# Performance work log

Measured on AMD Instinct MI355X. Metric: run time of the kernel, lower is better.

Reference implementation:

```python
import jax, jax.numpy as jnp
import numpy as np

B, L, D = 2, 2048, 2048
H, G, HD = 16, 4, 128
EPS = 1e-6
THETA_BASE = 10000.0


def setup_inputs() -> dict:
    key = jax.random.key(0)
    ks = jax.random.split(key, 5)
    x = jax.random.normal(ks[0], (B, L, D), jnp.float32)
    Wq = jax.random.normal(ks[1], (D, H * HD), jnp.float32) * 0.02
    Wk = jax.random.normal(ks[2], (D, G * HD), jnp.float32) * 0.02
    Wv = jax.random.normal(ks[3], (D, G * HD), jnp.float32) * 0.02
    Wo = jax.random.normal(ks[4], (H * HD, D), jnp.float32) * 0.02
    q_scale = jnp.ones((HD,), jnp.float32)
    k_scale = jnp.ones((HD,), jnp.float32)
    # Well-formed RoPE tables of shape [L, HD] (duplicated-half layout expected by apply_rope)
    inv_freq = 1.0 / (THETA_BASE ** (jnp.arange(0, HD // 2, dtype=jnp.float32) * 2.0 / HD))  # [HD/2]
    angles = jnp.arange(L, dtype=jnp.float32)[:, None] * inv_freq[None, :]  # [L, HD/2]
    angles = jnp.concatenate([angles, angles], axis=1)  # [L, HD]
    cos = jnp.cos(angles)
    sin = jnp.sin(angles)
    # Causal mask: True = masked (matches masked_fill(mask, -inf))
    mask = jnp.triu(jnp.ones((L, L), dtype=bool), k=1)
    return {"x": x, "Wq": Wq, "Wk": Wk, "Wv": Wv, "Wo": Wo,
            "q_scale": q_scale, "k_scale": k_scale, "cos": cos, "sin": sin, "mask": mask}


def _rmsnorm(x, scale):
    var = jnp.mean(x * x, axis=-1, keepdims=True)
    return x * jax.lax.rsqrt(var + EPS) * scale


def _rope(x, cos, sin):
    # x: [B, h, L, HD]; cos/sin: [L, HD]
    hd = x.shape[-1]
    x1, x2 = x[..., : hd // 2], x[..., hd // 2 :]
    rotated = jnp.concatenate([-x2, x1], axis=-1)
    return x * cos[None, None] + rotated * sin[None, None]


def reference(x, Wq, Wk, Wv, Wo, q_scale, k_scale, cos, sin, mask):
    b, l, _ = x.shape
    q = (x @ Wq).reshape(b, l, H, HD).transpose(0, 2, 1, 3)  # [B,H,L,HD]
    k = (x @ Wk).reshape(b, l, G, HD).transpose(0, 2, 1, 3)  # [B,G,L,HD]
    v = (x @ Wv).reshape(b, l, G, HD).transpose(0, 2, 1, 3)
    q = _rmsnorm(q, q_scale)
    k = _rmsnorm(k, k_scale)
    q = _rope(q, cos, sin)
    k = _rope(k, cos, sin)
    gs = H // G
    k = jnp.repeat(k, gs, axis=1)  # [B,H,L,HD]
    v = jnp.repeat(v, gs, axis=1)
    scores = jnp.einsum('bhqd,bhkd->bhqk', q, k)
    scores = jnp.where(mask, -jnp.inf, scores)
    # NB: faithful to the source's unusual scaling by head_dim**2 (not sqrt)
    w = jax.nn.softmax(scores / float(HD ** 2), axis=-1)
    out = jnp.einsum('bhqk,bhkd->bhqd', w, v).transpose(0, 2, 1, 3).reshape(b, l, H * HD)
    return out @ Wo
```

## Files before the change

### kernel.cpp

```cpp
#include <hip/hip_runtime.h>
#include <math.h>

#define SEQ 2048
#define DMODEL 2048
#define NHQ 16
#define NHK 4

typedef __attribute__((ext_vector_type(8))) short short8;
typedef __attribute__((ext_vector_type(8))) unsigned short ushort8;
typedef __attribute__((ext_vector_type(4))) float floatx4;

__device__ __forceinline__ unsigned short f2bf(float f) {
  unsigned int u = __builtin_bit_cast(unsigned int, f);
  u += 0x7fffu + ((u >> 16) & 1u);
  return (unsigned short)(u >> 16);
}
__device__ __forceinline__ float bf2f(unsigned short s) {
  unsigned int u = ((unsigned int)s) << 16;
  return __builtin_bit_cast(float, u);
}

__global__ __launch_bounds__(256) void prep(const float* __restrict__ x,
                                            const float* __restrict__ Wq,
                                            const float* __restrict__ Wk,
                                            const float* __restrict__ Wv,
                                            const float* __restrict__ Wo,
                                            unsigned short* __restrict__ x_bf,
                                            unsigned short* __restrict__ wqkv_t,
                                            unsigned short* __restrict__ wo_t) {
  const int z = blockIdx.z;
  const int tx = threadIdx.x, ty = threadIdx.y;
  const int tid = ty * 32 + tx;
  if (z == 3) {
    const size_t base = ((size_t)(blockIdx.y * 64 + blockIdx.x)) * 4096 + (size_t)tid * 16;
    const float4 v0 = *(const float4*)(x + base);
    const float4 v1 = *(const float4*)(x + base + 4);
    const float4 v2 = *(const float4*)(x + base + 8);
    const float4 v3 = *(const float4*)(x + base + 12);
    ushort8 w0, w1;
    w0[0] = f2bf(v0.x); w0[1] = f2bf(v0.y); w0[2] = f2bf(v0.z); w0[3] = f2bf(v0.w);
    w0[4] = f2bf(v1.x); w0[5] = f2bf(v1.y); w0[6] = f2bf(v1.z); w0[7] = f2bf(v1.w);
    w1[0] = f2bf(v2.x); w1[1] = f2bf(v2.y); w1[2] = f2bf(v2.z); w1[3] = f2bf(v2.w);
    w1[4] = f2bf(v3.x); w1[5] = f2bf(v3.y); w1[6] = f2bf(v3.z); w1[7] = f2bf(v3.w);
    *(ushort8*)(x_bf + base) = w0;
    *(ushort8*)(x_bf + base + 8) = w1;
    return;
  }
  int bx = blockIdx.x;
  const float* in;
  unsigned short* out;
  int C;
  const int R = 2048;
  if (z == 0)      { in = Wq; out = wqkv_t;                          C = 2048; }
  else if (z == 1) { in = Wo; out = wo_t;                            C = 2048; }
  else {
    if (bx < 16)      { in = Wk; out = wqkv_t + (size_t)2048 * 2048; C = 512; }
    else if (bx < 32) { in = Wv; out = wqkv_t + (size_t)2560 * 2048; C = 512; bx -= 16; }
    else return;
  }
  __shared__ float tile[32][65];
  const int c0 = bx * 32, r0 = blockIdx.y * 64;
#pragma unroll
  for (int j = 0; j < 8; ++j)
    tile[tx][ty + j * 8] = in[(size_t)(r0 + ty + j * 8) * C + c0 + tx];
  __syncthreads();
  const int c = tid >> 3;
  const int l8 = tid & 7;
  ushort8 w;
#pragma unroll
  for (int u = 0; u < 8; ++u) w[u] = f2bf(tile[c][l8 * 8 + u]);
  *(ushort8*)(out + (size_t)(c0 + c) * R + r0 + l8 * 8) = w;
}

__device__ __forceinline__ void stage_tile(const unsigned short* __restrict__ A,
                                           const unsigned short* __restrict__ Bt,
                                           unsigned short* As, unsigned short* Bs,
                                           int bm, int bn, int K, int k0,
                                           int wave, int srow, int scol) {
#pragma unroll
  for (int it = 0; it < 2; ++it) {
    const int rowa = wave * 32 + it * 16;
    const unsigned short* ga = A + (size_t)(bm + rowa + srow) * K + k0 + scol;
    const unsigned short* gb = Bt + (size_t)(bn + rowa + srow) * K + k0 + scol;
    __builtin_amdgcn_global_load_lds(
        (const __attribute__((address_space(1))) void*)ga,
        (__attribute__((address_space(3))) void*)&As[rowa * 32], 16, 0, 0);
    __builtin_amdgcn_global_load_lds(
        (const __attribute__((address_space(1))) void*)gb,
        (__attribute__((address_space(3))) void*)&Bs[rowa * 32], 16, 0, 0);
  }
}

__device__ __forceinline__ void mfma_tile(const unsigned short* As, const unsigned short* Bs,
                                          floatx4 (&acc)[4][4],
                                          int wr, int wc, int m15, int quad) {
  short8 af[4], bfr[4];
  const unsigned short* pa = &As[(wr * 64 + m15) * 32 + quad * 8];
  const unsigned short* pb = &Bs[(wc * 64 + m15) * 32 + quad * 8];
#pragma unroll
  for (int i = 0; i < 4; ++i) af[i] = *(const short8*)(pa + i * 16 * 32);
#pragma unroll
  for (int j = 0; j < 4; ++j) bfr[j] = *(const short8*)(pb + j * 16 * 32);
#pragma unroll
  for (int i = 0; i < 4; ++i)
#pragma unroll
    for (int j = 0; j < 4; ++j)
      acc[i][j] = __builtin_amdgcn_mfma_f32_16x16x32_bf16(af[i], bfr[j], acc[i][j], 0, 0, 0);
}

__global__ __launch_bounds__(256) void gemm_qkv_fused(const unsigned short* __restrict__ A,
                                                      const unsigned short* __restrict__ Bt,
                                                      unsigned short* __restrict__ qout,
                                                      unsigned short* __restrict__ kout,
                                                      unsigned short* __restrict__ vout,
                                                      const float* __restrict__ q_scale,
                                                      const float* __restrict__ k_scale,
                                                      const float* __restrict__ cosb,
                                                      const float* __restrict__ sinb) {
  __shared__ unsigned short smem[128 * 129];
  unsigned short* As0 = smem;
  unsigned short* Bs0 = smem + 4096;
  unsigned short* As1 = smem + 8192;
  unsigned short* Bs1 = smem + 12288;

  const int tid = threadIdx.x;
  const int wave = tid >> 6;
  const int lane = tid & 63;
  const int bm = blockIdx.y * 128;
  const int bx = blockIdx.x;
  const int bn = bx * 128;
  const int wr = wave >> 1;
  const int wc = wave & 1;
  const int m15 = lane & 15;
  const int quad = lane >> 4;

  floatx4 acc[4][4];
#pragma unroll
  for (int i = 0; i < 4; ++i)
#pragma unroll
    for (int j = 0; j < 4; ++j) acc[i][j] = (floatx4){0.f, 0.f, 0.f, 0.f};

  const int srow = lane >> 2;
  const int scol = (lane & 3) * 8;

  stage_tile(A, Bt, As0, Bs0, bm, bn, 2048, 0, wave, srow, scol);
  __syncthreads();

  for (int k0 = 0; k0 < 2048; k0 += 64) {
    stage_tile(A, Bt, As1, Bs1, bm, bn, 2048, k0 + 32, wave, srow, scol);
    mfma_tile(As0, Bs0, acc, wr, wc, m15, quad);
    __syncthreads();
    if (k0 + 64 < 2048)
      stage_tile(A, Bt, As0, Bs0, bm, bn, 2048, k0 + 64, wave, srow, scol);
    mfma_tile(As1, Bs1, acc, wr, wc, m15, quad);
    __syncthreads();
  }

#pragma unroll
  for (int i = 0; i < 4; ++i)
#pragma unroll
    for (int j = 0; j < 4; ++j) {
      const int col = wc * 64 + j * 16 + m15;
#pragma unroll
      for (int reg = 0; reg < 4; ++reg) {
        const int row = wr * 64 + i * 16 + quad * 4 + reg;
        smem[row * 129 + col] = f2bf(acc[i][j][reg]);
      }
    }
  __syncthreads();

  const int t = tid & 63;
  const int wv = tid >> 6;
  const int b = bm >> 11;
  const int l_base = bm & (SEQ - 1);

  if (bx < 20) {
    const float* scale = (bx < NHQ) ? q_scale : k_scale;
    unsigned short* dstbase = (bx < NHQ)
        ? qout + ((size_t)(b * NHQ + bx) * SEQ + l_base) * 128
        : kout + ((size_t)(b * NHK + (bx - NHQ)) * SEQ + l_base) * 128;
    const float sc0 = scale[t];
    const float sc1 = scale[t + 64];
#pragma unroll 4
    for (int rr = 0; rr < 32; ++rr) {
      const int row = wv * 32 + rr;
      const float v0 = bf2f(smem[row * 129 + t]);
      const float v1 = bf2f(smem[row * 129 + t + 64]);
      float ss = v0 * v0 + v1 * v1;
#pragma unroll
      for (int m = 1; m < 64; m <<= 1) ss += __shfl_xor(ss, m);
      const float r = rsqrtf(ss * (1.0f / 128.0f) + 1e-6f);
      const int l = l_base + row;
      const float c0 = cosb[(size_t)l * 128 + t];
      const float s0 = sinb[(size_t)l * 128 + t];
      const float c1 = cosb[(size_t)l * 128 + t + 64];
      const float s1 = sinb[(size_t)l * 128 + t + 64];
      const float a0 = v0 * r * sc0;
      const float a1 = v1 * r * sc1;
      unsigned short* dst = dstbase + (size_t)row * 128;
      dst[t]      = f2bf(a0 * c0 - a1 * s0);
      dst[t + 64] = f2bf(a1 * c1 + a0 * s1);
    }
  } else {
    const int g = bx - 20;
    unsigned short* vbase = vout + (size_t)(b * NHK + g) * 128 * SEQ + l_base;
#pragma unroll 4
    for (int dd = 0; dd < 32; ++dd) {
      const int d = wv * 32 + dd;
      unsigned short* dst = vbase + (size_t)d * SEQ;
      dst[t]      = smem[t * 129 + d];
      dst[t + 64] = smem[(t + 64) * 129 + d];
    }
  }
}

__global__ __launch_bounds__(256) void gemm_bf16_f32(const unsigned short* __restrict__ A,
                                                     const unsigned short* __restrict__ Bt,
                                                     float* __restrict__ C,
                                                     int M, int N, int K) {
  __shared__ unsigned short smem[4 * 128 * 32];
  unsigned short* As0 = smem;
  unsigned short* Bs0 = smem + 4096;
  unsigned short* As1 = smem + 8192;
  unsigned short* Bs1 = smem + 12288;

  const int tid = threadIdx.x;
  const int wave = tid >> 6;
  const int lane = tid & 63;
  const int bm = blockIdx.y * 128;
  const int bn = blockIdx.x * 128;
  const int wr = wave >> 1;
  const int wc = wave & 1;
  const int m15 = lane & 15;
  const int quad = lane >> 4;

  floatx4 acc[4][4];
#pragma unroll
  for (int i = 0; i < 4; ++i)
#pragma unroll
    for (int j = 0; j < 4; ++j) acc[i][j] = (floatx4){0.f, 0.f, 0.f, 0.f};

  const int srow = lane >> 2;
  const int scol = (lane & 3) * 8;

  stage_tile(A, Bt, As0, Bs0, bm, bn, K, 0, wave, srow, scol);
  __syncthreads();

  for (int k0 = 0; k0 < K; k0 += 64) {
    stage_tile(A, Bt, As1, Bs1, bm, bn, K, k0 + 32, wave, srow, scol);
    mfma_tile(As0, Bs0, acc, wr, wc, m15, quad);
    __syncthreads();
    if (k0 + 64 < K)
      stage_tile(A, Bt, As0, Bs0, bm, bn, K, k0 + 64, wave, srow, scol);
    mfma_tile(As1, Bs1, acc, wr, wc, m15, quad);
    __syncthreads();
  }

#pragma unroll
  for (int i = 0; i < 4; ++i)
#pragma unroll
    for (int j = 0; j < 4; ++j) {
      const int col = bn + wc * 64 + j * 16 + m15;
#pragma unroll
      for (int reg = 0; reg < 4; ++reg) {
        const int row = bm + wr * 64 + i * 16 + quad * 4 + reg;
        C[(size_t)row * N + col] = acc[i][j][reg];
      }
    }
}

__global__ __launch_bounds__(256, 4) void attn_mfma(const unsigned short* __restrict__ qb,
                                                    const unsigned short* __restrict__ kb,
                                                    const unsigned short* __restrict__ vtb,
                                                    unsigned short* __restrict__ o) {
  __shared__ unsigned short Ks[64 * 128];
  __shared__ unsigned short Vs[128 * 64];
  unsigned short* Ps = Ks;

  const int tid = threadIdx.x;
  const int wave = tid >> 6;
  const int lane = tid & 63;
  const int m15 = lane & 15;
  const int quad = lane >> 4;
  const int bh = blockIdx.x;
  const int b = bh >> 4;
  const int h = bh & 15;
  const int g = h >> 2;
  const int q0 = ((int)gridDim.y - 1 - (int)blockIdx.y) * 64;

  const unsigned short* qhead = qb + (size_t)bh * SEQ * 128;
  const unsigned short* khead = kb + (size_t)(b * NHK + g) * SEQ * 128;
  const unsigned short* vthead = vtb + (size_t)(b * NHK + g) * 128 * SEQ;

  short8 qf[4];
  {
    const unsigned short* qp = qhead + (size_t)(q0 + wave * 16 + m15) * 128 + quad * 8;
#pragma unroll
    for (int ks = 0; ks < 4; ++ks) qf[ks] = *(const short8*)(qp + ks * 32);
  }

  floatx4 acc_o[8];
#pragma unroll
  for (int n = 0; n < 8; ++n) acc_o[n] = (floatx4){0.f, 0.f, 0.f, 0.f};
  float l_lane[4] = {0.f, 0.f, 0.f, 0.f};
  const float inv_scale = 1.0f / 16384.0f;

  for (int j0 = 0; j0 <= q0; j0 += 64) {
#pragma unroll
    for (int t = 0; t < 4; ++t) {
      const int r = wave * 16 + t * 4 + (lane >> 4);
      const int cg = (lane & 15) ^ (r & 15);
      const unsigned short* src = khead + (size_t)(j0 + r) * 128 + cg * 8;
      __builtin_amdgcn_global_load_lds(
          (const __attribute__((address_space(1))) void*)src,
          (__attribute__((address_space(3))) void*)&Ks[(wave * 16 + t * 4) * 128], 16, 0, 0);
    }
#pragma unroll
    for (int t = 0; t < 4; ++t) {
      const int d = wave * 32 + t * 8 + (lane >> 3);
      const int cg = (lane & 7) ^ (d & 7);
      const unsigned short* src = vthead + (size_t)d * SEQ + j0 + cg * 8;
      __builtin_amdgcn_global_load_lds(
          (const __attribute__((address_space(1))) void*)src,
          (__attribute__((address_space(3))) void*)&Vs[(wave * 32 + t * 8) * 64], 16, 0, 0);
    }
    __syncthreads();

    floatx4 acc_s[4];
#pragma unroll
    for (int n = 0; n < 4; ++n) acc_s[n] = (floatx4){0.f, 0.f, 0.f, 0.f};
#pragma unroll
    for (int ks = 0; ks < 4; ++ks) {
#pragma unroll
      for (int n = 0; n < 4; ++n) {
        const short8 bfrag = *(const short8*)&Ks[(n * 16 + m15) * 128 + (((ks * 4 + quad) ^ m15) * 8)];
        acc_s[n] = __builtin_amdgcn_mfma_f32_16x16x32_bf16(qf[ks], bfrag, acc_s[n], 0, 0, 0);
      }
    }
    __syncthreads();

    if (j0 == q0) {
      const int row_g = wave * 16 + quad * 4;
#pragma unroll
      for (int n = 0; n < 4; ++n) {
        const int col = n * 16 + m15;
#pragma unroll
        for (int rg = 0; rg < 4; ++rg) {
          float p = (col > row_g + rg) ? 0.0f : __expf(acc_s[n][rg] * inv_scale);
          l_lane[rg] += p;
          Ps[(wave * 16 + quad * 4 + rg) * 72 + n * 16 + m15] = f2bf(p);
        }
      }
    } else {
#pragma unroll
      for (int n = 0; n < 4; ++n) {
#pragma unroll
        for (int rg = 0; rg < 4; ++rg) {
          const float p = __expf(acc_s[n][rg] * inv_scale);
          l_lane[rg] += p;
          Ps[(wave * 16 + quad * 4 + rg) * 72 + n * 16 + m15] = f2bf(p);
        }
      }
    }

#pragma unroll
    for (int kk = 0; kk < 2; ++kk) {
      const short8 a = *(const short8*)&Ps[(wave * 16 + m15) * 72 + kk * 32 + quad * 8];
#pragma unroll
      for (int n = 0; n < 8; ++n) {
        const short8 bfrag = *(const short8*)&Vs[(n * 16 + m15) * 64 + (((kk * 4 + quad) ^ (m15 & 7)) * 8)];
        acc_o[n] = __builtin_amdgcn_mfma_f32_16x16x32_bf16(a, bfrag, acc_o[n], 0, 0, 0);
      }
    }
    __syncthreads();
  }

#pragma unroll
  for (int rg = 0; rg < 4; ++rg) {
    float l = l_lane[rg];
    l += __shfl_xor(l, 1);
    l += __shfl_xor(l, 2);
    l += __shfl_xor(l, 4);
    l += __shfl_xor(l, 8);
    const float invl = 1.0f / l;
    const size_t row = (size_t)(b * SEQ + q0 + wave * 16 + quad * 4 + rg);
#pragma unroll
    for (int n = 0; n < 8; ++n)
      o[row * DMODEL + h * 128 + n * 16 + m15] = f2bf(acc_o[n][rg] * invl);
  }
}

extern "C" void kernel_launch(void* const* d_in, const int* in_sizes, int n_in,
                              void* d_out, int out_size, void* d_ws, size_t ws_size,
                              hipStream_t stream) {
  const float* x       = (const float*)d_in[0];
  const float* Wq      = (const float*)d_in[1];
  const float* Wk      = (const float*)d_in[2];
  const float* Wv      = (const float*)d_in[3];
  const float* Wo      = (const float*)d_in[4];
  const float* q_scale = (const float*)d_in[5];
  const float* k_scale = (const float*)d_in[6];
  const float* cosb    = (const float*)d_in[7];
  const float* sinb    = (const float*)d_in[8];
  float* out = (float*)d_out;

  char* w = (char*)d_ws;
  unsigned short* x_bf    = (unsigned short*)w;
  unsigned short* wqkv_t  = (unsigned short*)(w + 16777216);
  unsigned short* q_bf    = (unsigned short*)(w + 29360128);
  unsigned short* k_bf    = (unsigned short*)(w + 46137344);
  unsigned short* vt      = (unsigned short*)(w + 50331648);
  unsigned short* wo_t    = (unsigned short*)(w + 54525952);
  unsigned short* attn_bf = (unsigned short*)(w + 62914560);

  prep<<<dim3(64, 32, 4), dim3(32, 8), 0, stream>>>(x, Wq, Wk, Wv, Wo, x_bf, wqkv_t, wo_t);

  gemm_qkv_fused<<<dim3(24, 32), 256, 0, stream>>>(x_bf, wqkv_t, q_bf, k_bf, vt,
                                                   q_scale, k_scale, cosb, sinb);

  attn_mfma<<<dim3(2 * NHQ, SEQ / 64), 256, 0, stream>>>(q_bf, k_bf, vt, attn_bf);
  gemm_bf16_f32<<<dim3(2048 / 128, 4096 / 128), 256, 0, stream>>>(
      attn_bf, wo_t, out, 4096, 2048, 2048);
}
```

Measured before the change: 313.3 us.

## Use 8-wave GEMM blocks with XOR-swizzled LDS staging

Both bf16 GEMM kernels move from 4 waves to 8 waves per 128x128 tile, with each wave computing a 64x32 sub-tile and the QKV epilogue loops split over 8 waves. The global-to-LDS staging column is XOR-swizzled by row, and the MFMA fragment reads apply the matching swizzle to reduce LDS bank conflicts. The goal is more latency hiding and fewer LDS conflicts. The cost is more A-fragment re-reads per block and more barrier participants.

Measured after the change: 306.6 us. -2.2%, faster.

```diff
diff --git a/kernel.cpp b/kernel.cpp
--- a/kernel.cpp
+++ b/kernel.cpp
@@ -72,51 +72,49 @@
   *(ushort8*)(out + (size_t)(c0 + c) * R + r0 + l8 * 8) = w;
 }
 
-__device__ __forceinline__ void stage_tile(const unsigned short* __restrict__ A,
-                                           const unsigned short* __restrict__ Bt,
-                                           unsigned short* As, unsigned short* Bs,
-                                           int bm, int bn, int K, int k0,
-                                           int wave, int srow, int scol) {
-#pragma unroll
-  for (int it = 0; it < 2; ++it) {
-    const int rowa = wave * 32 + it * 16;
-    const unsigned short* ga = A + (size_t)(bm + rowa + srow) * K + k0 + scol;
-    const unsigned short* gb = Bt + (size_t)(bn + rowa + srow) * K + k0 + scol;
-    __builtin_amdgcn_global_load_lds(
-        (const __attribute__((address_space(1))) void*)ga,
-        (__attribute__((address_space(3))) void*)&As[rowa * 32], 16, 0, 0);
-    __builtin_amdgcn_global_load_lds(
-        (const __attribute__((address_space(1))) void*)gb,
-        (__attribute__((address_space(3))) void*)&Bs[rowa * 32], 16, 0, 0);
-  }
-}
-
-__device__ __forceinline__ void mfma_tile(const unsigned short* As, const unsigned short* Bs,
-                                          floatx4 (&acc)[4][4],
-                                          int wr, int wc, int m15, int quad) {
-  short8 af[4], bfr[4];
-  const unsigned short* pa = &As[(wr * 64 + m15) * 32 + quad * 8];
-  const unsigned short* pb = &Bs[(wc * 64 + m15) * 32 + quad * 8];
+__device__ __forceinline__ void stage_tile8(const unsigned short* __restrict__ A,
+                                            const unsigned short* __restrict__ Bt,
+                                            unsigned short* As, unsigned short* Bs,
+                                            int bm, int bn, int K, int k0,
+                                            int wave, int srow, int scol) {
+  const int rowa = wave * 16;
+  const unsigned short* ga = A + (size_t)(bm + rowa + srow) * K + k0 + scol;
+  const unsigned short* gb = Bt + (size_t)(bn + rowa + srow) * K + k0 + scol;
+  __builtin_amdgcn_global_load_lds(
+      (const __attribute__((address_space(1))) void*)ga,
+      (__attribute__((address_space(3))) void*)&As[rowa * 32], 16, 0, 0);
+  __builtin_amdgcn_global_load_lds(
+      (const __attribute__((address_space(1))) void*)gb,
+      (__attribute__((address_space(3))) void*)&Bs[rowa * 32], 16, 0, 0);
+}
+
+__device__ __forceinline__ void mfma_tile8(const unsigned short* As, const unsigned short* Bs,
+                                           floatx4 (&acc)[4][2],
+                                           int wr, int wc, int m15, int quad) {
+  const int co = ((quad ^ ((m15 >> 1) & 3)) * 8);
+  short8 af[4], bfr[2];
+  const unsigned short* pa = &As[(wr * 64 + m15) * 32 + co];
+  const unsigned short* pb = &Bs[(wc * 32 + m15) * 32 + co];
 #pragma unroll
   for (int i = 0; i < 4; ++i) af[i] = *(const short8*)(pa + i * 16 * 32);
 #pragma unroll
-  for (int j = 0; j < 4; ++j) bfr[j] = *(const short8*)(pb + j * 16 * 32);
+  for (int j = 0; j < 2; ++j) bfr[j] = *(const short8*)(pb + j * 16 * 32);
 #pragma unroll
   for (int i = 0; i < 4; ++i)
 #pragma unroll
-    for (int j = 0; j < 4; ++j)
+    for (int j = 0; j < 2; ++j)
       acc[i][j] = __builtin_amdgcn_mfma_f32_16x16x32_bf16(af[i], bfr[j], acc[i][j], 0, 0, 0);
 }
 
-__global__ __launch_bounds__(256) void gemm_qkv_fused(const unsigned short* __restrict__ A,
-                                                      const unsigned short* __restrict__ Bt,
-                                                      unsigned short* __restrict__ qout,
-                                                      unsigned short* __restrict__ kout,
-                                                      unsigned short* __restrict__ vout,
-                                                      const float* __restrict__ q_scale,
-                                                      const float* __restrict__ k_scale,
-                                                      const float* __restrict__ cosb,
-                                                      const float* __restrict__ sinb) {
+__global__ __launch_bounds__(512, 6) void gemm_qkv_fused(const unsigned short* __restrict__ A,
+                                                         const unsigned short* __restrict__ Bt,
+                                                         unsigned short* __restrict__ qout,
+                                                         unsigned short* __restrict__ kout,
+                                                         unsigned short* __restrict__ vout,
+                                                         const float* __restrict__ q_scale,
+                                                         const float* __restrict__ k_scale,
+                                                         const float* __restrict__ cosb,
+                                                         const float* __restrict__ sinb) {
   __shared__ unsigned short smem[128 * 129];
   unsigned short* As0 = smem;
   unsigned short* Bs0 = smem + 4096;
@@ -129,38 +127,38 @@
   const int bm = blockIdx.y * 128;
   const int bx = blockIdx.x;
   const int bn = bx * 128;
-  const int wr = wave >> 1;
-  const int wc = wave & 1;
+  const int wr = wave >> 2;
+  const int wc = wave & 3;
   const int m15 = lane & 15;
   const int quad = lane >> 4;
 
-  floatx4 acc[4][4];
+  floatx4 acc[4][2];
 #pragma unroll
   for (int i = 0; i < 4; ++i)
 #pragma unroll
-    for (int j = 0; j < 4; ++j) acc[i][j] = (floatx4){0.f, 0.f, 0.f, 0.f};
+    for (int j = 0; j < 2; ++j) acc[i][j] = (floatx4){0.f, 0.f, 0.f, 0.f};
 
   const int srow = lane >> 2;
-  const int scol = (lane & 3) * 8;
-
-  stage_tile(A, Bt, As0, Bs0, bm, bn, 2048, 0, wave, srow, scol);
+  const int scol = (((lane & 3) ^ ((lane >> 3) & 3))) * 8;
+
+  stage_tile8(A, Bt, As0, Bs0, bm, bn, 2048, 0, wave, srow, scol);
   __syncthreads();
 
   for (int k0 = 0; k0 < 2048; k0 += 64) {
-    stage_tile(A, Bt, As1, Bs1, bm, bn, 2048, k0 + 32, wave, srow, scol);
-    mfma_tile(As0, Bs0, acc, wr, wc, m15, quad);
+    stage_tile8(A, Bt, As1, Bs1, bm, bn, 2048, k0 + 32, wave, srow, scol);
+    mfma_tile8(As0, Bs0, acc, wr, wc, m15, quad);
     __syncthreads();
     if (k0 + 64 < 2048)
-      stage_tile(A, Bt, As0, Bs0, bm, bn, 2048, k0 + 64, wave, srow, scol);
-    mfma_tile(As1, Bs1, acc, wr, wc, m15, quad);
+      stage_tile8(A, Bt, As0, Bs0, bm, bn, 2048, k0 + 64, wave, srow, scol);
+    mfma_tile8(As1, Bs1, acc, wr, wc, m15, quad);
     __syncthreads();
   }
 
 #pragma unroll
   for (int i = 0; i < 4; ++i)
 #pragma unroll
-    for (int j = 0; j < 4; ++j) {
-      const int col = wc * 64 + j * 16 + m15;
+    for (int j = 0; j < 2; ++j) {
+      const int col = wc * 32 + j * 16 + m15;
 #pragma unroll
       for (int reg = 0; reg < 4; ++reg) {
         const int row = wr * 64 + i * 16 + quad * 4 + reg;
@@ -182,8 +180,8 @@
     const float sc0 = scale[t];
     const float sc1 = scale[t + 64];
 #pragma unroll 4
-    for (int rr = 0; rr < 32; ++rr) {
-      const int row = wv * 32 + rr;
+    for (int rr = 0; rr < 16; ++rr) {
+      const int row = wv * 16 + rr;
       const float v0 = bf2f(smem[row * 129 + t]);
       const float v1 = bf2f(smem[row * 129 + t + 64]);
       float ss = v0 * v0 + v1 * v1;
@@ -205,8 +203,8 @@
     const int g = bx - 20;
     unsigned short* vbase = vout + (size_t)(b * NHK + g) * 128 * SEQ + l_base;
 #pragma unroll 4
-    for (int dd = 0; dd < 32; ++dd) {
-      const int d = wv * 32 + dd;
+    for (int dd = 0; dd < 16; ++dd) {
+      const int d = wv * 16 + dd;
       unsigned short* dst = vbase + (size_t)d * SEQ;
       dst[t]      = smem[t * 129 + d];
       dst[t + 64] = smem[(t + 64) * 129 + d];
@@ -214,10 +212,10 @@
   }
 }
 
-__global__ __launch_bounds__(256) void gemm_bf16_f32(const unsigned short* __restrict__ A,
-                                                     const unsigned short* __restrict__ Bt,
-                                                     float* __restrict__ C,
-                                                     int M, int N, int K) {
+__global__ __launch_bounds__(512, 6) void gemm_bf16_f32(const unsigned short* __restrict__ A,
+                                                        const unsigned short* __restrict__ Bt,
+                                                        float* __restrict__ C,
+                                                        int M, int N, int K) {
   __shared__ unsigned short smem[4 * 128 * 32];
   unsigned short* As0 = smem;
   unsigned short* Bs0 = smem + 4096;
@@ -229,38 +227,38 @@
   const int lane = tid & 63;
   const int bm = blockIdx.y * 128;
   const int bn = blockIdx.x * 128;
-  const int wr = wave >> 1;
-  const int wc = wave & 1;
+  const int wr = wave >> 2;
+  const int wc = wave & 3;
   const int m15 = lane & 15;
   const int quad = lane >> 4;
 
-  floatx4 acc[4][4];
+  floatx4 acc[4][2];
 #pragma unroll
   for (int i = 0; i < 4; ++i)
 #pragma unroll
-    for (int j = 0; j < 4; ++j) acc[i][j] = (floatx4){0.f, 0.f, 0.f, 0.f};
+    for (int j = 0; j < 2; ++j) acc[i][j] = (floatx4){0.f, 0.f, 0.f, 0.f};
 
   const int srow = lane >> 2;
-  const int scol = (lane & 3) * 8;
-
-  stage_tile(A, Bt, As0, Bs0, bm, bn, K, 0, wave, srow, scol);
+  const int scol = (((lane & 3) ^ ((lane >> 3) & 3))) * 8;
+
+  stage_tile8(A, Bt, As0, Bs0, bm, bn, K, 0, wave, srow, scol);
   __syncthreads();
 
   for (int k0 = 0; k0 < K; k0 += 64) {
-    stage_tile(A, Bt, As1, Bs1, bm, bn, K, k0 + 32, wave, srow, scol);
-    mfma_tile(As0, Bs0, acc, wr, wc, m15, quad);
+    stage_tile8(A, Bt, As1, Bs1, bm, bn, K, k0 + 32, wave, srow, scol);
+    mfma_tile8(As0, Bs0, acc, wr, wc, m15, quad);
     __syncthreads();
     if (k0 + 64 < K)
-      stage_tile(A, Bt, As0, Bs0, bm, bn, K, k0 + 64, wave, srow, scol);
-    mfma_tile(As1, Bs1, acc, wr, wc, m15, quad);
+      stage_tile8(A, Bt, As0, Bs0, bm, bn, K, k0 + 64, wave, srow, scol);
+    mfma_tile8(As1, Bs1, acc, wr, wc, m15, quad);
     __syncthreads();
   }
 
 #pragma unroll
   for (int i = 0; i < 4; ++i)
 #pragma unroll
-    for (int j = 0; j < 4; ++j) {
-      const int col = bn + wc * 64 + j * 16 + m15;
+    for (int j = 0; j < 2; ++j) {
+      const int col = bn + wc * 32 + j * 16 + m15;
 #pragma unroll
       for (int reg = 0; reg < 4; ++reg) {
         const int row = bm + wr * 64 + i * 16 + quad * 4 + reg;
@@ -415,10 +413,10 @@
 
   prep<<<dim3(64, 32, 4), dim3(32, 8), 0, stream>>>(x, Wq, Wk, Wv, Wo, x_bf, wqkv_t, wo_t);
 
-  gemm_qkv_fused<<<dim3(24, 32), 256, 0, stream>>>(x_bf, wqkv_t, q_bf, k_bf, vt,
+  gemm_qkv_fused<<<dim3(24, 32), 512, 0, stream>>>(x_bf, wqkv_t, q_bf, k_bf, vt,
                                                    q_scale, k_scale, cosb, sinb);
 
   attn_mfma<<<dim3(2 * NHQ, SEQ / 64), 256, 0, stream>>>(q_bf, k_bf, vt, attn_bf);
-  gemm_bf16_f32<<<dim3(2048 / 128, 4096 / 128), 256, 0, stream>>>(
+  gemm_bf16_f32<<<dim3(2048 / 128, 4096 / 128), 512, 0, stream>>>(
       attn_bf, wo_t, out, 4096, 2048, 2048);
 }
```

## Use 256x256 tiles with 8 waves and a pipelined, swizzled k-loop for GEMMs

Applied to the files above, without the earlier changes.

Both GEMMs (the fused QKV projection and the output projection) move from 128x128 tiles with 4 waves to 256x256 tiles with 8 waves. They share a new k-loop that triple-buffers loads in LDS with a swizzled layout, interleaves global-to-LDS loads with MFMA groups, and uses explicit vmcnt waits, sched barriers and setprio. The QKV epilogue is split into two head-sized passes so it still fits in LDS. The aim is more data reuse per LDS byte and better overlap of memory traffic with MFMA work. In exchange the grids get much smaller (192 and 128 blocks), which risks underfilling the CUs, and register and LDS pressure goes up.

Result: slower. 332.5 us (+6.1%).

```diff
diff --git a/kernel.cpp b/kernel.cpp
--- a/kernel.cpp
+++ b/kernel.cpp
@@ -9,6 +9,9 @@
 typedef __attribute__((ext_vector_type(8))) short short8;
 typedef __attribute__((ext_vector_type(8))) unsigned short ushort8;
 typedef __attribute__((ext_vector_type(4))) float floatx4;
+
+#define AS1 __attribute__((address_space(1)))
+#define AS3 __attribute__((address_space(3)))
 
 __device__ __forceinline__ unsigned short f2bf(float f) {
   unsigned int u = __builtin_bit_cast(unsigned int, f);
@@ -72,201 +75,255 @@
   *(ushort8*)(out + (size_t)(c0 + c) * R + r0 + l8 * 8) = w;
 }
 
-__device__ __forceinline__ void stage_tile(const unsigned short* __restrict__ A,
-                                           const unsigned short* __restrict__ Bt,
-                                           unsigned short* As, unsigned short* Bs,
-                                           int bm, int bn, int K, int k0,
-                                           int wave, int srow, int scol) {
-#pragma unroll
-  for (int it = 0; it < 2; ++it) {
-    const int rowa = wave * 32 + it * 16;
-    const unsigned short* ga = A + (size_t)(bm + rowa + srow) * K + k0 + scol;
-    const unsigned short* gb = Bt + (size_t)(bn + rowa + srow) * K + k0 + scol;
-    __builtin_amdgcn_global_load_lds(
-        (const __attribute__((address_space(1))) void*)ga,
-        (__attribute__((address_space(3))) void*)&As[rowa * 32], 16, 0, 0);
-    __builtin_amdgcn_global_load_lds(
-        (const __attribute__((address_space(1))) void*)gb,
-        (__attribute__((address_space(3))) void*)&Bs[rowa * 32], 16, 0, 0);
-  }
-}
-
-__device__ __forceinline__ void mfma_tile(const unsigned short* As, const unsigned short* Bs,
-                                          floatx4 (&acc)[4][4],
-                                          int wr, int wc, int m15, int quad) {
-  short8 af[4], bfr[4];
-  const unsigned short* pa = &As[(wr * 64 + m15) * 32 + quad * 8];
-  const unsigned short* pb = &Bs[(wc * 64 + m15) * 32 + quad * 8];
-#pragma unroll
-  for (int i = 0; i < 4; ++i) af[i] = *(const short8*)(pa + i * 16 * 32);
-#pragma unroll
-  for (int j = 0; j < 4; ++j) bfr[j] = *(const short8*)(pb + j * 16 * 32);
+#define PBAR() do { __builtin_amdgcn_sched_barrier(0); __builtin_amdgcn_s_barrier(); \
+                    __builtin_amdgcn_sched_barrier(0); } while (0)
+#define KWAIT(deep) do { if (deep) asm volatile("s_waitcnt vmcnt(8)" ::: "memory"); \
+                         else      asm volatile("s_waitcnt vmcnt(0)" ::: "memory"); } while (0)
+
+__device__ __forceinline__ void mfma_q(floatx4 (&ac)[4][4],
+                                       const short8 (&a)[4], const short8 (&b)[4]) {
 #pragma unroll
   for (int i = 0; i < 4; ++i)
 #pragma unroll
     for (int j = 0; j < 4; ++j)
-      acc[i][j] = __builtin_amdgcn_mfma_f32_16x16x32_bf16(af[i], bfr[j], acc[i][j], 0, 0, 0);
-}
-
-__global__ __launch_bounds__(256) void gemm_qkv_fused(const unsigned short* __restrict__ A,
-                                                      const unsigned short* __restrict__ Bt,
-                                                      unsigned short* __restrict__ qout,
-                                                      unsigned short* __restrict__ kout,
-                                                      unsigned short* __restrict__ vout,
-                                                      const float* __restrict__ q_scale,
-                                                      const float* __restrict__ k_scale,
-                                                      const float* __restrict__ cosb,
-                                                      const float* __restrict__ sinb) {
-  __shared__ unsigned short smem[128 * 129];
-  unsigned short* As0 = smem;
-  unsigned short* Bs0 = smem + 4096;
-  unsigned short* As1 = smem + 8192;
-  unsigned short* Bs1 = smem + 12288;
+      ac[i][j] = __builtin_amdgcn_mfma_f32_16x16x32_bf16(a[i], b[j], ac[i][j], 0, 0, 0);
+}
+
+__device__ __forceinline__ void ld4(short8 (&v)[4], const unsigned short* p) {
+#pragma unroll
+  for (int i = 0; i < 4; ++i) v[i] = *(const short8*)(p + i * 512);
+}
+
+__device__ __forceinline__ void stg_half(const unsigned short* src0,
+                                         unsigned short* dst_uniform) {
+  __builtin_amdgcn_global_load_lds((const AS1 void*)src0,
+                                   (AS3 void*)dst_uniform, 16, 0, 0);
+  __builtin_amdgcn_global_load_lds((const AS1 void*)(src0 + (size_t)128 * 2048),
+                                   (AS3 void*)(dst_uniform + 4096), 16, 0, 0);
+}
+
+__device__ __forceinline__ void kloop256(const unsigned short* __restrict__ A,
+                                         const unsigned short* __restrict__ Bt,
+                                         unsigned short* ldsA, unsigned short* ldsB,
+                                         int bm, int bn, int tid,
+                                         floatx4 (&accL)[4][4], floatx4 (&accH)[4][4]) {
+  const int wave = tid >> 6;
+  const int lane = tid & 63;
+  const int m15 = lane & 15;
+  const int quad = lane >> 4;
+  const int wr = wave >> 2;
+  const int wcol = wave & 3;
+
+  const int srow = tid >> 2;
+  const int csrc = ((tid & 3) ^ (srow & 3)) * 8;
+  const unsigned short* gA = A + (size_t)(bm + srow) * 2048 + csrc;
+  const unsigned short* gB = Bt + (size_t)(bn + srow) * 2048 + csrc;
+  const int wslot = wave * 512;
+
+  const int aoff = (wr * 128 + m15) * 32 + (quad ^ (m15 & 3)) * 8;
+  const int boff = (wcol * 64 + m15) * 32 + (quad ^ (m15 & 3)) * 8;
+
+  stg_half(gA + 0,  ldsA + wslot);
+  stg_half(gB + 0,  ldsB + wslot);
+  stg_half(gA + 32, ldsA + 8192 + wslot);
+  stg_half(gB + 32, ldsB + 8192 + wslot);
+  stg_half(gA + 64, ldsA + 16384 + wslot);
+  stg_half(gB + 64, ldsB + 16384 + wslot);
+  asm volatile("s_waitcnt vmcnt(0)" ::: "memory");
+  __builtin_amdgcn_s_barrier();
+  __builtin_amdgcn_sched_barrier(0);
+
+  const int NK = 32;
+  short8 af[4], bv[4];
+  for (int t = 0; t < NK; ++t) {
+    const int d = t & 1;
+    unsigned short* Ab0 = ldsA + d * 16384;
+    unsigned short* Bb0 = ldsB + d * 16384;
+    unsigned short* Aalt = ldsA + (d ^ 1) * 16384;
+    unsigned short* Balt = ldsB + (d ^ 1) * 16384;
+    const bool st1 = (t + 1 < NK), st2 = (t + 2 < NK);
+    const int k1 = (t + 1) * 64 + 32;
+    const int k2 = (t + 2) * 64;
+
+    ld4(af, Ab0 + aoff);
+    ld4(bv, Bb0 + boff);
+    if (st1) stg_half(gA + k1, Aalt + 8192 + wslot);
+    PBAR();
+    __builtin_amdgcn_s_setprio(1);
+    mfma_q(accL, af, bv);
+    __builtin_amdgcn_s_setprio(0);
+    PBAR();
+
+    ld4(af, Ab0 + aoff + 2048);
+    if (st1) stg_half(gB + k1, Balt + 8192 + wslot);
+    PBAR();
+    __builtin_amdgcn_s_setprio(1);
+    mfma_q(accH, af, bv);
+    __builtin_amdgcn_s_setprio(0);
+    KWAIT(st2);
+    PBAR();
+
+    ld4(af, Ab0 + 8192 + aoff);
+    ld4(bv, Bb0 + 8192 + boff);
+    if (st2) stg_half(gA + k2, Ab0 + wslot);
+    PBAR();
+    __builtin_amdgcn_s_setprio(1);
+    mfma_q(accL, af, bv);
+    __builtin_amdgcn_s_setprio(0);
+    PBAR();
+
+    ld4(af, Ab0 + 8192 + aoff + 2048);
+    if (st2) stg_half(gB + k2, Bb0 + wslot);
+    PBAR();
+    __builtin_amdgcn_s_setprio(1);
+    mfma_q(accH, af, bv);
+    __builtin_amdgcn_s_setprio(0);
+    KWAIT(st2);
+    PBAR();
+  }
+}
+
+__global__ __launch_bounds__(512, 2) void gemm_qkv_fused(const unsigned short* __restrict__ A,
+                                                         const unsigned short* __restrict__ Bt,
+                                                         unsigned short* __restrict__ qout,
+                                                         unsigned short* __restrict__ kout,
+                                                         unsigned short* __restrict__ vout,
+                                                         const float* __restrict__ q_scale,
+                                                         const float* __restrict__ k_scale,
+                                                         const float* __restrict__ cosb,
+                                                         const float* __restrict__ sinb) {
+  __shared__ unsigned short lds[65536];
+  unsigned short* ldsA = lds;
+  unsigned short* ldsB = lds + 32768;
 
   const int tid = threadIdx.x;
   const int wave = tid >> 6;
   const int lane = tid & 63;
-  const int bm = blockIdx.y * 128;
-  const int bx = blockIdx.x;
-  const int bn = bx * 128;
-  const int wr = wave >> 1;
-  const int wc = wave & 1;
   const int m15 = lane & 15;
   const int quad = lane >> 4;
-
-  floatx4 acc[4][4];
+  const int wr = wave >> 2;
+  const int wcol = wave & 3;
+  const int bxn = blockIdx.x;
+  const int bm = blockIdx.y * 256;
+  const int bn = bxn * 256;
+
+  floatx4 accL[4][4], accH[4][4];
 #pragma unroll
   for (int i = 0; i < 4; ++i)
 #pragma unroll
-    for (int j = 0; j < 4; ++j) acc[i][j] = (floatx4){0.f, 0.f, 0.f, 0.f};
-
-  const int srow = lane >> 2;
-  const int scol = (lane & 3) * 8;
-
-  stage_tile(A, Bt, As0, Bs0, bm, bn, 2048, 0, wave, srow, scol);
-  __syncthreads();
-
-  for (int k0 = 0; k0 < 2048; k0 += 64) {
-    stage_tile(A, Bt, As1, Bs1, bm, bn, 2048, k0 + 32, wave, srow, scol);
-    mfma_tile(As0, Bs0, acc, wr, wc, m15, quad);
-    __syncthreads();
-    if (k0 + 64 < 2048)
-      stage_tile(A, Bt, As0, Bs0, bm, bn, 2048, k0 + 64, wave, srow, scol);
-    mfma_tile(As1, Bs1, acc, wr, wc, m15, quad);
-    __syncthreads();
-  }
-
-#pragma unroll
-  for (int i = 0; i < 4; ++i)
-#pragma unroll
     for (int j = 0; j < 4; ++j) {
-      const int col = wc * 64 + j * 16 + m15;
-#pragma unroll
-      for (int reg = 0; reg < 4; ++reg) {
-        const int row = wr * 64 + i * 16 + quad * 4 + reg;
-        smem[row * 129 + col] = f2bf(acc[i][j][reg]);
-      }
-    }
-  __syncthreads();
-
-  const int t = tid & 63;
-  const int wv = tid >> 6;
+      accL[i][j] = (floatx4){0.f, 0.f, 0.f, 0.f};
+      accH[i][j] = (floatx4){0.f, 0.f, 0.f, 0.f};
+    }
+
+  kloop256(A, Bt, ldsA, ldsB, bm, bn, tid, accL, accH);
+
+  unsigned short* epi = lds;
   const int b = bm >> 11;
   const int l_base = bm & (SEQ - 1);
-
-  if (bx < 20) {
-    const float* scale = (bx < NHQ) ? q_scale : k_scale;
-    unsigned short* dstbase = (bx < NHQ)
-        ? qout + ((size_t)(b * NHQ + bx) * SEQ + l_base) * 128
-        : kout + ((size_t)(b * NHK + (bx - NHQ)) * SEQ + l_base) * 128;
-    const float sc0 = scale[t];
-    const float sc1 = scale[t + 64];
+  const int t64 = tid & 63;
+
+  for (int c = 0; c < 2; ++c) {
+    __syncthreads();
+    if ((wcol >> 1) == c) {
+      const int colb = (wcol & 1) * 64;
+#pragma unroll
+      for (int i = 0; i < 4; ++i)
+#pragma unroll
+        for (int j = 0; j < 4; ++j)
+#pragma unroll
+          for (int r = 0; r < 4; ++r) {
+            epi[(wr * 128 + i * 16 + quad * 4 + r) * 129 + colb + j * 16 + m15] =
+                f2bf(accL[i][j][r]);
+            epi[(wr * 128 + 64 + i * 16 + quad * 4 + r) * 129 + colb + j * 16 + m15] =
+                f2bf(accH[i][j][r]);
+          }
+    }
+    __syncthreads();
+
+    const int hh = 2 * bxn + c;
+    if (hh < 20) {
+      const float* scale = (hh < NHQ) ? q_scale : k_scale;
+      unsigned short* dstbase = (hh < NHQ)
+          ? qout + ((size_t)(b * NHQ + hh) * SEQ + l_base) * 128
+          : kout + ((size_t)(b * NHK + (hh - NHQ)) * SEQ + l_base) * 128;
+      const float sc0 = scale[t64];
+      const float sc1 = scale[t64 + 64];
 #pragma unroll 4
-    for (int rr = 0; rr < 32; ++rr) {
-      const int row = wv * 32 + rr;
-      const float v0 = bf2f(smem[row * 129 + t]);
-      const float v1 = bf2f(smem[row * 129 + t + 64]);
-      float ss = v0 * v0 + v1 * v1;
-#pragma unroll
-      for (int m = 1; m < 64; m <<= 1) ss += __shfl_xor(ss, m);
-      const float r = rsqrtf(ss * (1.0f / 128.0f) + 1e-6f);
-      const int l = l_base + row;
-      const float c0 = cosb[(size_t)l * 128 + t];
-      const float s0 = sinb[(size_t)l * 128 + t];
-      const float c1 = cosb[(size_t)l * 128 + t + 64];
-      const float s1 = sinb[(size_t)l * 128 + t + 64];
-      const float a0 = v0 * r * sc0;
-      const float a1 = v1 * r * sc1;
-      unsigned short* dst = dstbase + (size_t)row * 128;
-      dst[t]      = f2bf(a0 * c0 - a1 * s0);
-      dst[t + 64] = f2bf(a1 * c1 + a0 * s1);
-    }
-  } else {
-    const int g = bx - 20;
-    unsigned short* vbase = vout + (size_t)(b * NHK + g) * 128 * SEQ + l_base;
+      for (int rr = 0; rr < 32; ++rr) {
+        const int row = wave * 32 + rr;
+        const float v0 = bf2f(epi[row * 129 + t64]);
+        const float v1 = bf2f(epi[row * 129 + t64 + 64]);
+        float ss = v0 * v0 + v1 * v1;
+#pragma unroll
+        for (int m = 1; m < 64; m <<= 1) ss += __shfl_xor(ss, m);
+        const float r = rsqrtf(ss * (1.0f / 128.0f) + 1e-6f);
+        const int l = l_base + row;
+        const float c0v = cosb[(size_t)l * 128 + t64];
+        const float s0 = sinb[(size_t)l * 128 + t64];
+        const float c1v = cosb[(size_t)l * 128 + t64 + 64];
+        const float s1 = sinb[(size_t)l * 128 + t64 + 64];
+        const float a0 = v0 * r * sc0;
+        const float a1 = v1 * r * sc1;
+        unsigned short* dst = dstbase + (size_t)row * 128;
+        dst[t64]      = f2bf(a0 * c0v - a1 * s0);
+        dst[t64 + 64] = f2bf(a1 * c1v + a0 * s1);
+      }
+    } else {
+      const int g = hh - 20;
+      unsigned short* vbase = vout + (size_t)(b * NHK + g) * 128 * SEQ + l_base;
 #pragma unroll 4
-    for (int dd = 0; dd < 32; ++dd) {
-      const int d = wv * 32 + dd;
-      unsigned short* dst = vbase + (size_t)d * SEQ;
-      dst[t]      = smem[t * 129 + d];
-      dst[t + 64] = smem[(t + 64) * 129 + d];
-    }
-  }
-}
-
-__global__ __launch_bounds__(256) void gemm_bf16_f32(const unsigned short* __restrict__ A,
-                                                     const unsigned short* __restrict__ Bt,
-                                                     float* __restrict__ C,
-                                                     int M, int N, int K) {
-  __shared__ unsigned short smem[4 * 128 * 32];
-  unsigned short* As0 = smem;
-  unsigned short* Bs0 = smem + 4096;
-  unsigned short* As1 = smem + 8192;
-  unsigned short* Bs1 = smem + 12288;
+      for (int dd = 0; dd < 16; ++dd) {
+        const int d = wave * 16 + dd;
+        unsigned short* dst = vbase + (size_t)d * SEQ;
+        dst[t64]       = epi[t64 * 129 + d];
+        dst[t64 + 64]  = epi[(t64 + 64) * 129 + d];
+        dst[t64 + 128] = epi[(t64 + 128) * 129 + d];
+        dst[t64 + 192] = epi[(t64 + 192) * 129 + d];
+      }
+    }
+  }
+}
+
+__global__ __launch_bounds__(512, 2) void gemm_bf16_f32(const unsigned short* __restrict__ A,
+                                                        const unsigned short* __restrict__ Bt,
+                                                        float* __restrict__ C,
+                                                        int M, int N, int K) {
+  __shared__ unsigned short lds[65536];
+  unsigned short* ldsA = lds;
+  unsigned short* ldsB = lds + 32768;
 
   const int tid = threadIdx.x;
   const int wave = tid >> 6;
   const int lane = tid & 63;
-  const int bm = blockIdx.y * 128;
-  const int bn = blockIdx.x * 128;
-  const int wr = wave >> 1;
-  const int wc = wave & 1;
   const int m15 = lane & 15;
   const int quad = lane >> 4;
-
-  floatx4 acc[4][4];
+  const int wr = wave >> 2;
+  const int wcol = wave & 3;
+  const int bm = blockIdx.y * 256;
+  const int bn = blockIdx.x * 256;
+
+  floatx4 accL[4][4], accH[4][4];
 #pragma unroll
   for (int i = 0; i < 4; ++i)
 #pragma unroll
-    for (int j = 0; j < 4; ++j) acc[i][j] = (floatx4){0.f, 0.f, 0.f, 0.f};
-
-  const int srow = lane >> 2;
-  const int scol = (lane & 3) * 8;
-
-  stage_tile(A, Bt, As0, Bs0, bm, bn, K, 0, wave, srow, scol);
-  __syncthreads();
-
-  for (int k0 = 0; k0 < K; k0 += 64) {
-    stage_tile(A, Bt, As1, Bs1, bm, bn, K, k0 + 32, wave, srow, scol);
-    mfma_tile(As0, Bs0, acc, wr, wc, m15, quad);
-    __syncthreads();
-    if (k0 + 64 < K)
-      stage_tile(A, Bt, As0, Bs0, bm, bn, K, k0 + 64, wave, srow, scol);
-    mfma_tile(As1, Bs1, acc, wr, wc, m15, quad);
-    __syncthreads();
-  }
+    for (int j = 0; j < 4; ++j) {
+      accL[i][j] = (floatx4){0.f, 0.f, 0.f, 0.f};
+      accH[i][j] = (floatx4){0.f, 0.f, 0.f, 0.f};
+    }
+
+  kloop256(A, Bt, ldsA, ldsB, bm, bn, tid, accL, accH);
 
 #pragma unroll
   for (int i = 0; i < 4; ++i)
 #pragma unroll
-    for (int j = 0; j < 4; ++j) {
-      const int col = bn + wc * 64 + j * 16 + m15;
-#pragma unroll
-      for (int reg = 0; reg < 4; ++reg) {
-        const int row = bm + wr * 64 + i * 16 + quad * 4 + reg;
-        C[(size_t)row * N + col] = acc[i][j][reg];
-      }
-    }
+    for (int j = 0; j < 4; ++j)
+#pragma unroll
+      for (int r = 0; r < 4; ++r) {
+        const int col = bn + wcol * 64 + j * 16 + m15;
+        C[(size_t)(bm + wr * 128 + i * 16 + quad * 4 + r) * N + col] = accL[i][j][r];
+        C[(size_t)(bm + wr * 128 + 64 + i * 16 + quad * 4 + r) * N + col] = accH[i][j][r];
+      }
 }
 
 __global__ __launch_bounds__(256, 4) void attn_mfma(const unsigned short* __restrict__ qb,
@@ -312,8 +369,8 @@
       const int cg = (lane & 15) ^ (r & 15);
       const unsigned short* src = khead + (size_t)(j0 + r) * 128 + cg * 8;
       __builtin_amdgcn_global_load_lds(
-          (const __attribute__((address_space(1))) void*)src,
-          (__attribute__((address_space(3))) void*)&Ks[(wave * 16 + t * 4) * 128], 16, 0, 0);
+          (const AS1 void*)src,
+          (AS3 void*)&Ks[(wave * 16 + t * 4) * 128], 16, 0, 0);
     }
 #pragma unroll
     for (int t = 0; t < 4; ++t) {
@@ -321,8 +378,8 @@
       const int cg = (lane & 7) ^ (d & 7);
       const unsigned short* src = vthead + (size_t)d * SEQ + j0 + cg * 8;
       __builtin_amdgcn_global_load_lds(
-          (const __attribute__((address_space(1))) void*)src,
-          (__attribute__((address_space(3))) void*)&Vs[(wave * 32 + t * 8) * 64], 16, 0, 0);
+          (const AS1 void*)src,
+          (AS3 void*)&Vs[(wave * 32 + t * 8) * 64], 16, 0, 0);
     }
     __syncthreads();
 
@@ -415,10 +472,11 @@
 
   prep<<<dim3(64, 32, 4), dim3(32, 8), 0, stream>>>(x, Wq, Wk, Wv, Wo, x_bf, wqkv_t, wo_t);
 
-  gemm_qkv_fused<<<dim3(24, 32), 256, 0, stream>>>(x_bf, wqkv_t, q_bf, k_bf, vt,
+  gemm_qkv_fused<<<dim3(12, 16), 512, 0, stream>>>(x_bf, wqkv_t, q_bf, k_bf, vt,
                                                    q_scale, k_scale, cosb, sinb);
 
   attn_mfma<<<dim3(2 * NHQ, SEQ / 64), 256, 0, stream>>>(q_bf, k_bf, vt, attn_bf);
-  gemm_bf16_f32<<<dim3(2048 / 128, 4096 / 128), 256, 0, stream>>>(
+
+  gemm_bf16_f32<<<dim3(2048 / 256, 4096 / 256), 512, 0, stream>>>(
       attn_bf, wo_t, out, 4096, 2048, 2048);
 }
```
